# Performance work log

Hardware: AMD Instinct MI355X
Metric: run time of the kernel (lower is better)

The kernel has to match this reference:

```python
import jax, jax.numpy as jnp
import numpy as np

E, D, H, K, DIL, T = 8, 768, 3072, 3, 1, 16384


def _conv1d(x, w, b, dilation):
    # x: [1, C_in, L]; w: [C_out, C_in, K]; torch Conv1d with SAME padding
    pad = dilation * (w.shape[-1] - 1) // 2
    y = jax.lax.conv_general_dilated(
        x, w, window_strides=(1,), padding=[(pad, pad)],
        rhs_dilation=(dilation,), dimension_numbers=("NCH", "OIH", "NCH"))
    return y + b[None, :, None]


def setup_inputs() -> dict:
    key = jax.random.key(0)
    k0, k1, k2, k3, k4 = jax.random.split(key, 5)
    inp = jax.random.normal(k0, (T, D), dtype=jnp.float32)
    fwd_expert_count = jnp.full((E,), T // E, dtype=jnp.int32)
    w1 = jax.random.normal(k1, (E, H, D, K), dtype=jnp.float32) * (1.0 / np.sqrt(D * K))
    b1 = jax.random.normal(k2, (E, H), dtype=jnp.float32) * 0.01
    w2 = jax.random.normal(k3, (E, D, H, K), dtype=jnp.float32) * (1.0 / np.sqrt(H * K))
    b2 = jax.random.normal(k4, (E, D), dtype=jnp.float32) * 0.01
    return {"inp": inp, "fwd_expert_count": fwd_expert_count,
            "w1": w1, "b1": b1, "w2": w2, "b2": b2}


def reference(inp, fwd_expert_count, w1, b1, w2, b2):
    # counts define static per-expert segment lengths (constants w.r.t. compute graph)
    counts = np.asarray(jax.device_get(fwd_expert_count))
    x = inp.T[None]  # [1, D, T]
    outs, idx = [], 0
    for i in range(counts.shape[0]):
        n = int(counts[i])
        if n > 0:
            outs.append(_conv1d(x[:, :, idx:idx + n], w1[i], b1[i], DIL))
            idx += n
    h = jax.nn.gelu(jnp.concatenate(outs, axis=2), approximate=False)  # [1, H, T]
    outs, idx = [], 0
    for i in range(counts.shape[0]):
        n = int(counts[i])
        if n > 0:
            outs.append(_conv1d(h[:, :, idx:idx + n], w2[i], b2[i], DIL))
            idx += n
    y = jnp.concatenate(outs, axis=2)[0]  # [D, T]
    return y.T  # [T, D]
```

## Files before the change

kernel.cpp:

```cpp
#include <hip/hip_runtime.h>
#include <hip/hip_bf16.h>
#include <cstdint>

#define E_   8
#define D_   768
#define H_   3072
#define T_   16384
#define SEG  2048
#define PSEG (SEG + 2)

typedef __attribute__((ext_vector_type(8))) __bf16 bf16x8;
typedef __attribute__((ext_vector_type(4))) float f32x4;
typedef __attribute__((ext_vector_type(4))) unsigned int u32x4;

__device__ inline unsigned short f2bf(float f) {
  union { float f; unsigned int u; } v; v.f = f;
  unsigned int u = v.u;
  u += 0x7fffu + ((u >> 16) & 1u);
  return (unsigned short)(u >> 16);
}

__device__ inline float gelu_fast(float x) {
  const float a = -2.302118131f;
  const float b = -0.102944213f;
  float z = x * __builtin_fmaf(b, x * x, a);
  float e = __builtin_amdgcn_exp2f(z);
  return x * __builtin_amdgcn_rcpf(1.0f + e);
}

__device__ inline unsigned cvt_pk_bf16(float lo, float hi) {
  unsigned r;
  asm("v_cvt_pk_bf16_f32 %0, %1, %2" : "=v"(r) : "v"(lo), "v"(hi));
  return r;
}

__device__ inline void gload16(const unsigned short* g, unsigned short* l) {
  __builtin_amdgcn_global_load_lds(
      (const __attribute__((address_space(1))) unsigned int*)g,
      (__attribute__((address_space(3))) unsigned int*)l, 16, 0, 0);
}

__global__ __launch_bounds__(256) void cvt_x_pad_kernel(const float* __restrict__ in,
                                                        unsigned short* __restrict__ out) {
  const int i = blockIdx.x * 256 + threadIdx.x;
  const int elem = i * 8;
  const int row = elem / D_;
  const int col = elem - row * D_;
  const int prow = (row >> 11) * PSEG + 1 + (row & (SEG - 1));
  const float* p = in + (size_t)row * D_ + col;
  u32x4 v;
#pragma unroll
  for (int j = 0; j < 4; ++j)
    v[j] = (unsigned)f2bf(p[2 * j]) | ((unsigned)f2bf(p[2 * j + 1]) << 16);
  *(u32x4*)(out + (size_t)prow * D_ + col) = v;
}

__global__ __launch_bounds__(256) void zero_guards2_kernel(unsigned short* __restrict__ Xp,
                                                           unsigned short* __restrict__ Hp) {
  const int b = blockIdx.x;
  unsigned short* buf = (b < 16) ? Xp : Hp;
  const int C = (b < 16) ? D_ : H_;
  const int bb = b & 15;
  const int e = bb >> 1;
  const size_t row = (size_t)e * PSEG + (bb & 1) * (PSEG - 1);
  for (int c = threadIdx.x; c < C; c += 256) buf[row * C + c] = 0;
}

template <int C>
__global__ __launch_bounds__(256) void cvt_w_kernel(const float* __restrict__ in,
                                                    unsigned short* __restrict__ out) {
  constexpr int C8 = C / 8;
  const int i = blockIdx.x * 256 + threadIdx.x;
  const int row = i / C8;
  const int cq = i - row * C8;
  const float* src = in + ((size_t)row * C + cq * 8) * 3;
  unsigned short* dst = out + (size_t)row * 3 * C + cq * 8;
  f32x4 v[6];
#pragma unroll
  for (int j = 0; j < 6; ++j) v[j] = *(const f32x4*)(src + j * 4);
  const float* f = (const float*)v;
#pragma unroll
  for (int k = 0; k < 3; ++k) {
    u32x4 w;
#pragma unroll
    for (int j = 0; j < 4; ++j)
      w[j] = (unsigned)f2bf(f[(2 * j) * 3 + k]) |
             ((unsigned)f2bf(f[(2 * j + 1) * 3 + k]) << 16);
    *(u32x4*)(dst + k * C) = w;
  }
}

template <int CIN, int COUT, bool DO_GELU>
__global__ __launch_bounds__(512, 2) void conv_gemm8_kernel(
    const unsigned short* __restrict__ A,
    const unsigned short* __restrict__ Bt,
    const float* __restrict__ bias,
    void* __restrict__ Out) {
  __shared__ __align__(16) unsigned short lds[65536];

  constexpr int CSTEPS = CIN / 64;
  constexpr int NT = 3 * CSTEPS;
  constexpr int NTN = COUT / 256;

  const int tid  = threadIdx.x;
  const int wid  = tid >> 6, lane = tid & 63;
  const int wm   = wid >> 2, wn = wid & 3;

  const int bid = blockIdx.x;
  const int e   = bid & 7;
  const int rem = bid >> 3;
  const int mc  = rem / (4 * NTN);
  const int r2  = rem - mc * 4 * NTN;
  const int m0  = (mc * 4 + (r2 & 3)) * 256;
  const int n0  = (r2 >> 2) * 256;

  const int rowoff = tid >> 3;
  const int psrc   = ((lane & 7) ^ (lane >> 3)) * 8;
  const int ko     = (lane >> 4) * 16;
  const int ax     = (lane & 7) << 4;
  const int l15    = lane & 15;

  const int koax0 = ko ^ ax;
  const int koax1 = (64 | ko) ^ ax;
  const char* pA0 = (const char*)lds + wm * 16384 + l15 * 128 + koax0;
  const char* pA1 = (const char*)lds + wm * 16384 + l15 * 128 + koax1;
  const char* pB0 = (const char*)lds + 65536 + (wn >> 1) * 16384 +
                    ((wn & 1) * 64 + l15) * 128 + koax0;
  const char* pB1 = (const char*)lds + 65536 + (wn >> 1) * 16384 +
                    ((wn & 1) * 64 + l15) * 128 + koax1;

  const unsigned short* aU = A + ((size_t)e * PSEG + m0) * CIN;
  const unsigned short* bU = Bt + (size_t)(e * COUT + n0) * 3 * CIN;
  const int avo = rowoff * CIN + psrc;
  const int bvo = rowoff * 3 * CIN + psrc;
  size_t aOff = 0, bOff = 0;

  f32x4 acc[8][4];
#pragma unroll
  for (int n = 0; n < 4; ++n) {
    const float bv = bias[e * COUT + n0 + wn * 64 + n * 16 + l15];
#pragma unroll
    for (int m = 0; m < 8; ++m) acc[m][n] = (f32x4){bv, bv, bv, bv};
  }

#define STAGE_A(BUF_, part_) do {                                                    \
    _Pragma("unroll")                                                                \
    for (int ii_ = 0; ii_ < 2; ++ii_)                                                \
      gload16(aU + aOff + avo + (ii_ * 128 + (part_) * 64) * CIN,                    \
              (unsigned short*)((char*)lds + (BUF_) * 32768 + ii_ * 16384 +          \
                                (part_) * 8192 + wid * 1024 + lane * 16));           \
  } while (0)

#define STAGE_B(BUF_, h_) do {                                                       \
    _Pragma("unroll")                                                                \
    for (int ii_ = 0; ii_ < 2; ++ii_)                                                \
      gload16(bU + bOff + bvo + ((h_) * 128 + ii_ * 64) * 3 * CIN,                   \
              (unsigned short*)((char*)lds + 65536 + (BUF_) * 32768 + (h_) * 16384 + \
                                ii_ * 8192 + wid * 1024 + lane * 16));               \
  } while (0)

#define ADVA(nx_) do { if ((nx_) < NT) aOff += 64; } while (0)
#define ADVB(nx_) do { if ((nx_) < NT) bOff += 64; } while (0)

#define FULLBAR() do { asm volatile("" ::: "memory");                                \
                       __builtin_amdgcn_s_barrier();                                 \
                       asm volatile("" ::: "memory"); } while (0)
#define VM6() asm volatile("s_waitcnt vmcnt(6)" ::: "memory")
#define VM4() asm volatile("s_waitcnt vmcnt(4)" ::: "memory")
#define VM_NONE()

#define RA(buf_, mq_, s_, raA_, raB_, RB_) do {                                      \
    const char* pAx_ = (s_) ? pA1 : pA0;                                             \
    if (RB_) {                                                                       \
      const char* pBx_ = (s_) ? pB1 : pB0;                                           \
      _Pragma("unroll")                                                              \
      for (int n_ = 0; n_ < 4; ++n_)                                                 \
        raB_[n_] = *(const bf16x8*)(pBx_ + (buf_) * 32768 + n_ * 2048);              \
    }                                                                                \
    _Pragma("unroll")                                                                \
    for (int mi_ = 0; mi_ < 4; ++mi_)                                                \
      raA_[mi_] = *(const bf16x8*)(pAx_ + (buf_) * 32768 + ((mq_) * 4 + mi_) * 2048);\
  } while (0)

#define PHASE(raBuf_, raMq_, raS_, raA_, raB_, RB_, useA_, useB_, mq_, STAGE_STMT, VMW_) \
  do {                                                                               \
    FULLBAR();                                                                       \
    RA(raBuf_, raMq_, raS_, raA_, raB_, RB_);                                        \
    STAGE_STMT;                                                                      \
    __builtin_amdgcn_s_setprio(1);                                                   \
    _Pragma("unroll")                                                                \
    for (int mi_ = 0; mi_ < 4; ++mi_)                                                \
      _Pragma("unroll")                                                              \
      for (int n_ = 0; n_ < 4; ++n_)                                                 \
        acc[(mq_) * 4 + mi_][n_] = __builtin_amdgcn_mfma_f32_16x16x32_bf16(          \
            useA_[mi_], useB_[n_], acc[(mq_) * 4 + mi_][n_], 0, 0, 0);               \
    __builtin_amdgcn_s_setprio(0);                                                   \
    VMW_();                                                                          \
  } while (0)

  STAGE_B(0, 0); STAGE_B(0, 1); ADVB(1);
  STAGE_A(0, 0); STAGE_A(0, 1); ADVA(1);
  STAGE_B(1, 0); STAGE_B(1, 1); ADVB(2);
  VM6();
  FULLBAR();

  bf16x8 aFA[4], aFB[4], bFA[4], bFB[4];
  RA(0, 0, 0, aFA, bFA, 1);

  int kt0 = 0;
#pragma unroll 1
  for (int it = 0; it < NT / 2; ++it, kt0 += 2) {
    PHASE(0, 0, 1, aFB, bFB, 1, aFA, bFA, 0, STAGE_A(1, 0), VM6);
    PHASE(0, 1, 0, aFA, bFA, 0, aFB, bFB, 0, { STAGE_A(1, 1); ADVA(kt0 + 2); }, VM_NONE);
    PHASE(0, 1, 1, aFB, bFB, 0, aFA, bFA, 1, STAGE_B(0, 0), VM4);
    PHASE(1, 0, 0, aFA, bFA, 1, aFB, bFB, 1, { STAGE_B(0, 1); ADVB(kt0 + 3); }, VM_NONE);
    PHASE(1, 0, 1, aFB, bFB, 1, aFA, bFA, 0, STAGE_A(0, 0), VM6);
    PHASE(1, 1, 0, aFA, bFA, 0, aFB, bFB, 0, { STAGE_A(0, 1); ADVA(kt0 + 3); }, VM_NONE);
    PHASE(1, 1, 1, aFB, bFB, 0, aFA, bFA, 1, STAGE_B(1, 0), VM4);
    PHASE(0, 0, 0, aFA, bFA, 1, aFB, bFB, 1, { STAGE_B(1, 1); ADVB(kt0 + 4); }, VM_NONE);
  }

  asm volatile("s_waitcnt vmcnt(0)" ::: "memory");

#undef PHASE
#undef RA
#undef STAGE_A
#undef STAGE_B
#undef ADVA
#undef ADVB

#pragma unroll
  for (int m = 0; m < 8; ++m) {
    const int rowb = m0 + wm * 128 + m * 16 + ((lane >> 4) << 2);
#pragma unroll
    for (int n = 0; n < 4; ++n) {
      const int col = n0 + wn * 64 + n * 16 + l15;
      if (DO_GELU) {
        unsigned short* ob = (unsigned short*)Out +
                             ((size_t)e * PSEG + 1 + rowb) * COUT + col;
#pragma unroll
        for (int i = 0; i < 4; i += 2) {
          const unsigned pk = cvt_pk_bf16(gelu_fast(acc[m][n][i]),
                                          gelu_fast(acc[m][n][i + 1]));
          ob[(size_t)i * COUT] = (unsigned short)pk;
          ob[(size_t)(i + 1) * COUT] = (unsigned short)(pk >> 16);
        }
      } else {
        float* ob = (float*)Out + ((size_t)e * SEG + rowb) * COUT + col;
#pragma unroll
        for (int i = 0; i < 4; ++i) ob[(size_t)i * COUT] = acc[m][n][i];
      }
    }
  }
#undef FULLBAR
#undef VM6
#undef VM4
#undef VM_NONE
}

template <int CIN, int COUT>
__global__ __launch_bounds__(512, 2) void conv_gemm_n192_kernel(
    const unsigned short* __restrict__ A,
    const unsigned short* __restrict__ Bt,
    const float* __restrict__ bias,
    float* __restrict__ Out) {
  __shared__ __align__(16) unsigned short lds[57344];

  constexpr int CSTEPS = CIN / 64;
  constexpr int NT = 3 * CSTEPS;

  const int tid  = threadIdx.x;
  const int wid  = tid >> 6, lane = tid & 63;
  const int wm   = wid >> 2, wn = wid & 3;

  const int bid = blockIdx.x;
  const int e   = bid & 7;
  const int rem = bid >> 3;
  const int m0  = (rem & 7) * 256;
  const int n0  = (rem >> 3) * 192;

  const int rowoff = tid >> 3;
  const int psrc   = ((lane & 7) ^ (lane >> 3)) * 8;
  const int ko     = (lane >> 4) * 16;
  const int ax     = (lane & 7) << 4;
  const int l15    = lane & 15;

  const int koax0 = ko ^ ax;
  const int koax1 = (64 | ko) ^ ax;
  const char* pA0 = (const char*)lds + wm * 16384 + l15 * 128 + koax0;
  const char* pA1 = (const char*)lds + wm * 16384 + l15 * 128 + koax1;
  const char* pB0 = (const char*)lds + 65536 + wn * 6144 + l15 * 128 + koax0;
  const char* pB1 = (const char*)lds + 65536 + wn * 6144 + l15 * 128 + koax1;

  const unsigned short* aU = A + ((size_t)e * PSEG + m0) * CIN;
  const unsigned short* bU = Bt + (size_t)(e * COUT + n0) * 3 * CIN;
  const int avo = rowoff * CIN + psrc;
  const int bvo = rowoff * 3 * CIN + psrc;
  size_t aOff = 0, bOff = 0;

  f32x4 acc[8][3];
#pragma unroll
  for (int n = 0; n < 3; ++n) {
    const float bv = bias[e * COUT + n0 + wn * 48 + n * 16 + l15];
#pragma unroll
    for (int m = 0; m < 8; ++m) acc[m][n] = (f32x4){bv, bv, bv, bv};
  }

#define ADVA(nx_) do { if ((nx_) < NT) aOff += 64; } while (0)
#define ADVB(nx_) do { if ((nx_) < NT) bOff += 64; } while (0)

#define STAGE_A2(BUF_, slot_)                                                        \
  gload16(aU + aOff + avo + ((slot_) * 64) * CIN,                                    \
          (unsigned short*)((char*)lds + (BUF_) * 32768 + (slot_) * 8192 +           \
                            wid * 1024 + lane * 16))
#define STAGE_B2(BUF_, slot_)                                                        \
  gload16(bU + bOff + bvo + ((slot_) * 64) * 3 * CIN,                                \
          (unsigned short*)((char*)lds + 65536 + (BUF_) * 24576 + (slot_) * 8192 +   \
                            wid * 1024 + lane * 16))

#define FULLBAR() do { asm volatile("" ::: "memory");                                \
                       __builtin_amdgcn_s_barrier();                                 \
                       asm volatile("" ::: "memory"); } while (0)
#define VM3() asm volatile("s_waitcnt vmcnt(3)" ::: "memory")
#define VM2() asm volatile("s_waitcnt vmcnt(2)" ::: "memory")

#define RA_A2(buf_, mq_, s_, dst_) do {                                              \
    const char* pAx_ = (s_) ? pA1 : pA0;                                             \
    _Pragma("unroll")                                                                \
    for (int mi_ = 0; mi_ < 4; ++mi_)                                                \
      dst_[mi_] = *(const bf16x8*)(pAx_ + (buf_) * 32768 + ((mq_) * 4 + mi_) * 2048);\
  } while (0)

#define RA_B2(buf_, s_, dst_) do {                                                   \
    const char* pBx_ = (s_) ? pB1 : pB0;                                             \
    _Pragma("unroll")                                                                \
    for (int n_ = 0; n_ < 3; ++n_)                                                   \
      dst_[n_] = *(const bf16x8*)(pBx_ + (buf_) * 24576 + n_ * 2048);                \
  } while (0)

#define MFMA12(mq_, aU_, bU_) do {                                                   \
    __builtin_amdgcn_s_setprio(1);                                                   \
    _Pragma("unroll")                                                                \
    for (int mi_ = 0; mi_ < 4; ++mi_)                                                \
      _Pragma("unroll")                                                              \
      for (int n_ = 0; n_ < 3; ++n_)                                                 \
        acc[(mq_) * 4 + mi_][n_] = __builtin_amdgcn_mfma_f32_16x16x32_bf16(          \
            aU_[mi_], bU_[n_], acc[(mq_) * 4 + mi_][n_], 0, 0, 0);                   \
    __builtin_amdgcn_s_setprio(0);                                                   \
  } while (0)

  STAGE_A2(0, 0); STAGE_A2(0, 1); STAGE_A2(0, 2); STAGE_A2(0, 3); ADVA(1);
  STAGE_B2(0, 0); STAGE_B2(0, 1); STAGE_B2(0, 2); ADVB(1);
  STAGE_B2(1, 0); STAGE_B2(1, 1); STAGE_B2(1, 2); ADVB(2);
  VM3();
  FULLBAR();

  bf16x8 aX[4], aY[4], bF0[3], bF1[3];
  RA_A2(0, 0, 0, aX);
  RA_B2(0, 0, bF0);

  int kt0 = 0;
#pragma unroll 1
  for (int it = 0; it < NT / 2; ++it, kt0 += 2) {
    FULLBAR(); RA_A2(0, 0, 1, aY); RA_B2(0, 1, bF1);
               STAGE_A2(1, 0); STAGE_A2(1, 1); STAGE_A2(1, 2); STAGE_A2(1, 3);
               ADVA(kt0 + 2); MFMA12(0, aX, bF0);
    FULLBAR(); RA_A2(0, 1, 0, aX); MFMA12(0, aY, bF1);
    FULLBAR(); RA_A2(0, 1, 1, aY); STAGE_B2(0, 0); STAGE_B2(0, 1);
               MFMA12(1, aX, bF0); VM2();
    FULLBAR(); RA_A2(1, 0, 0, aX); RA_B2(1, 0, bF0); STAGE_B2(0, 2);
               ADVB(kt0 + 3); MFMA12(1, aY, bF1);
    FULLBAR(); RA_A2(1, 0, 1, aY); RA_B2(1, 1, bF1);
               STAGE_A2(0, 0); STAGE_A2(0, 1); STAGE_A2(0, 2); STAGE_A2(0, 3);
               ADVA(kt0 + 3); MFMA12(0, aX, bF0);
    FULLBAR(); RA_A2(1, 1, 0, aX); MFMA12(0, aY, bF1);
    FULLBAR(); RA_A2(1, 1, 1, aY); STAGE_B2(1, 0); STAGE_B2(1, 1);
               MFMA12(1, aX, bF0); VM2();
    FULLBAR(); RA_A2(0, 0, 0, aX); RA_B2(0, 0, bF0); STAGE_B2(1, 2);
               ADVB(kt0 + 4); MFMA12(1, aY, bF1);
  }

  asm volatile("s_waitcnt vmcnt(0)" ::: "memory");

#undef MFMA12
#undef RA_A2
#undef RA_B2
#undef STAGE_A2
#undef STAGE_B2
#undef ADVA
#undef ADVB
#undef FULLBAR
#undef VM3
#undef VM2

#pragma unroll
  for (int m = 0; m < 8; ++m) {
    const int rowb = m0 + wm * 128 + m * 16 + ((lane >> 4) << 2);
#pragma unroll
    for (int n = 0; n < 3; ++n) {
      const int col = n0 + wn * 48 + n * 16 + l15;
      float* ob = Out + ((size_t)e * SEG + rowb) * COUT + col;
#pragma unroll
      for (int i = 0; i < 4; ++i) ob[(size_t)i * COUT] = acc[m][n][i];
    }
  }
}

extern "C" void kernel_launch(void* const* d_in, const int* in_sizes, int n_in,
                              void* d_out, int out_size, void* d_ws, size_t ws_size,
                              hipStream_t stream) {
  const float* inp = (const float*)d_in[0];
  const float* w1 = (const float*)d_in[2];
  const float* b1 = (const float*)d_in[3];
  const float* w2 = (const float*)d_in[4];
  const float* b2 = (const float*)d_in[5];
  float* out = (float*)d_out;
  char* ws = (char*)d_ws;

  const size_t szXp = (size_t)E_ * PSEG * D_ * 2;
  const size_t szHp = (size_t)E_ * PSEG * H_ * 2;
  const size_t szW1 = (size_t)E_ * H_ * 3 * D_ * 2;
  const size_t szW2 = (size_t)E_ * D_ * 3 * H_ * 2;

  unsigned short* Xp  = (unsigned short*)ws;
  unsigned short* Hp  = (unsigned short*)(ws + szXp);
  unsigned short* W1T = (unsigned short*)(ws + szXp + szHp);
  unsigned short* W2T = (unsigned short*)(ws + szXp + szHp + szW1);

  if (ws_size < szXp + szHp + szW1 + szW2) return;

  zero_guards2_kernel<<<32, 256, 0, stream>>>(Xp, Hp);
  cvt_x_pad_kernel<<<T_ * D_ / 8 / 256, 256, 0, stream>>>(inp, Xp);
  cvt_w_kernel<D_><<<(E_ * H_) * (D_ / 8) / 256, 256, 0, stream>>>(w1, W1T);
  cvt_w_kernel<H_><<<(E_ * D_) * (H_ / 8) / 256, 256, 0, stream>>>(w2, W2T);

  constexpr int NWG1 = (H_ / 256) * (SEG / 256) * E_;
  constexpr int NWG2 = (D_ / 192) * (SEG / 256) * E_;
  conv_gemm8_kernel<D_, H_, true>
      <<<NWG1, 512, 0, stream>>>(Xp, W1T, b1, Hp);
  conv_gemm_n192_kernel<H_, D_>
      <<<NWG2, 512, 0, stream>>>(Hp, W2T, b2, out);
}
```

Measured before the change: 513.3 us.

## Switch conv GEMMs from 8-wave to 4-wave blocks with larger per-wave tiles

Result: slower. 724.4 us (+41.1%).

```diff
diff --git a/kernel.cpp b/kernel.cpp
--- a/kernel.cpp
+++ b/kernel.cpp
@@ -91,7 +91,7 @@
 }
 
 template <int CIN, int COUT, bool DO_GELU>
-__global__ __launch_bounds__(512, 2) void conv_gemm8_kernel(
+__global__ __launch_bounds__(256, 1) void conv_gemm4_kernel(
     const unsigned short* __restrict__ A,
     const unsigned short* __restrict__ Bt,
     const float* __restrict__ bias,
@@ -104,7 +104,7 @@
 
   const int tid  = threadIdx.x;
   const int wid  = tid >> 6, lane = tid & 63;
-  const int wm   = wid >> 2, wn = wid & 3;
+  const int wm   = wid >> 1, wn = wid & 1;
 
   const int bid = blockIdx.x;
   const int e   = bid & 7;
@@ -124,10 +124,8 @@
   const int koax1 = (64 | ko) ^ ax;
   const char* pA0 = (const char*)lds + wm * 16384 + l15 * 128 + koax0;
   const char* pA1 = (const char*)lds + wm * 16384 + l15 * 128 + koax1;
-  const char* pB0 = (const char*)lds + 65536 + (wn >> 1) * 16384 +
-                    ((wn & 1) * 64 + l15) * 128 + koax0;
-  const char* pB1 = (const char*)lds + 65536 + (wn >> 1) * 16384 +
-                    ((wn & 1) * 64 + l15) * 128 + koax1;
+  const char* pB0 = (const char*)lds + 65536 + wn * 16384 + l15 * 128 + koax0;
+  const char* pB1 = (const char*)lds + 65536 + wn * 16384 + l15 * 128 + koax1;
 
   const unsigned short* aU = A + ((size_t)e * PSEG + m0) * CIN;
   const unsigned short* bU = Bt + (size_t)(e * COUT + n0) * 3 * CIN;
@@ -135,10 +133,10 @@
   const int bvo = rowoff * 3 * CIN + psrc;
   size_t aOff = 0, bOff = 0;
 
-  f32x4 acc[8][4];
-#pragma unroll
-  for (int n = 0; n < 4; ++n) {
-    const float bv = bias[e * COUT + n0 + wn * 64 + n * 16 + l15];
+  f32x4 acc[8][8];
+#pragma unroll
+  for (int n = 0; n < 8; ++n) {
+    const float bv = bias[e * COUT + n0 + wn * 128 + n * 16 + l15];
 #pragma unroll
     for (int m = 0; m < 8; ++m) acc[m][n] = (f32x4){bv, bv, bv, bv};
   }
@@ -146,17 +144,23 @@
 #define STAGE_A(BUF_, part_) do {                                                    \
     _Pragma("unroll")                                                                \
     for (int ii_ = 0; ii_ < 2; ++ii_)                                                \
-      gload16(aU + aOff + avo + (ii_ * 128 + (part_) * 64) * CIN,                    \
-              (unsigned short*)((char*)lds + (BUF_) * 32768 + ii_ * 16384 +          \
-                                (part_) * 8192 + wid * 1024 + lane * 16));           \
+      _Pragma("unroll")                                                              \
+      for (int j_ = 0; j_ < 2; ++j_)                                                 \
+        gload16(aU + aOff + avo + (ii_ * 128 + (part_) * 64 + j_ * 32) * CIN,        \
+                (unsigned short*)((char*)lds + (BUF_) * 32768 + ii_ * 16384 +        \
+                                  (part_) * 8192 + j_ * 4096 + wid * 1024 +          \
+                                  lane * 16));                                       \
   } while (0)
 
 #define STAGE_B(BUF_, h_) do {                                                       \
     _Pragma("unroll")                                                                \
     for (int ii_ = 0; ii_ < 2; ++ii_)                                                \
-      gload16(bU + bOff + bvo + ((h_) * 128 + ii_ * 64) * 3 * CIN,                   \
-              (unsigned short*)((char*)lds + 65536 + (BUF_) * 32768 + (h_) * 16384 + \
-                                ii_ * 8192 + wid * 1024 + lane * 16));               \
+      _Pragma("unroll")                                                              \
+      for (int j_ = 0; j_ < 2; ++j_)                                                 \
+        gload16(bU + bOff + bvo + ((h_) * 128 + ii_ * 64 + j_ * 32) * 3 * CIN,       \
+                (unsigned short*)((char*)lds + 65536 + (BUF_) * 32768 +              \
+                                  (h_) * 16384 + ii_ * 8192 + j_ * 4096 +            \
+                                  wid * 1024 + lane * 16));                          \
   } while (0)
 
 #define ADVA(nx_) do { if ((nx_) < NT) aOff += 64; } while (0)
@@ -165,35 +169,36 @@
 #define FULLBAR() do { asm volatile("" ::: "memory");                                \
                        __builtin_amdgcn_s_barrier();                                 \
                        asm volatile("" ::: "memory"); } while (0)
-#define VM6() asm volatile("s_waitcnt vmcnt(6)" ::: "memory")
-#define VM4() asm volatile("s_waitcnt vmcnt(4)" ::: "memory")
+#define VMA() asm volatile("s_waitcnt vmcnt(12)" ::: "memory")
+#define VMB() asm volatile("s_waitcnt vmcnt(8)" ::: "memory")
 #define VM_NONE()
 
-#define RA(buf_, mq_, s_, raA_, raB_, RB_) do {                                      \
+#define RA(buf_, mh_, s_, raA_, raB_, RB_) do {                                      \
     const char* pAx_ = (s_) ? pA1 : pA0;                                             \
     if (RB_) {                                                                       \
       const char* pBx_ = (s_) ? pB1 : pB0;                                           \
       _Pragma("unroll")                                                              \
-      for (int n_ = 0; n_ < 4; ++n_)                                                 \
+      for (int n_ = 0; n_ < 8; ++n_)                                                 \
         raB_[n_] = *(const bf16x8*)(pBx_ + (buf_) * 32768 + n_ * 2048);              \
     }                                                                                \
     _Pragma("unroll")                                                                \
     for (int mi_ = 0; mi_ < 4; ++mi_)                                                \
-      raA_[mi_] = *(const bf16x8*)(pAx_ + (buf_) * 32768 + ((mq_) * 4 + mi_) * 2048);\
-  } while (0)
-
-#define PHASE(raBuf_, raMq_, raS_, raA_, raB_, RB_, useA_, useB_, mq_, STAGE_STMT, VMW_) \
+      raA_[mi_] = *(const bf16x8*)(pAx_ + (buf_) * 32768 + (mh_) * 8192 +            \
+                                   mi_ * 2048);                                      \
+  } while (0)
+
+#define PHASE(raBuf_, raMh_, raS_, raA_, raB_, RB_, useA_, useB_, mh_, STAGE_STMT, VMW_) \
   do {                                                                               \
     FULLBAR();                                                                       \
-    RA(raBuf_, raMq_, raS_, raA_, raB_, RB_);                                        \
+    RA(raBuf_, raMh_, raS_, raA_, raB_, RB_);                                        \
     STAGE_STMT;                                                                      \
     __builtin_amdgcn_s_setprio(1);                                                   \
     _Pragma("unroll")                                                                \
     for (int mi_ = 0; mi_ < 4; ++mi_)                                                \
       _Pragma("unroll")                                                              \
-      for (int n_ = 0; n_ < 4; ++n_)                                                 \
-        acc[(mq_) * 4 + mi_][n_] = __builtin_amdgcn_mfma_f32_16x16x32_bf16(          \
-            useA_[mi_], useB_[n_], acc[(mq_) * 4 + mi_][n_], 0, 0, 0);               \
+      for (int n_ = 0; n_ < 8; ++n_)                                                 \
+        acc[(mh_) * 4 + mi_][n_] = __builtin_amdgcn_mfma_f32_16x16x32_bf16(          \
+            useA_[mi_], useB_[n_], acc[(mh_) * 4 + mi_][n_], 0, 0, 0);               \
     __builtin_amdgcn_s_setprio(0);                                                   \
     VMW_();                                                                          \
   } while (0)
@@ -201,23 +206,23 @@
   STAGE_B(0, 0); STAGE_B(0, 1); ADVB(1);
   STAGE_A(0, 0); STAGE_A(0, 1); ADVA(1);
   STAGE_B(1, 0); STAGE_B(1, 1); ADVB(2);
-  VM6();
+  VMA();
   FULLBAR();
 
-  bf16x8 aFA[4], aFB[4], bFA[4], bFB[4];
-  RA(0, 0, 0, aFA, bFA, 1);
+  bf16x8 aX[4], aY[4], bF0[8], bF1[8];
+  RA(0, 0, 0, aX, bF0, 1);
 
   int kt0 = 0;
 #pragma unroll 1
   for (int it = 0; it < NT / 2; ++it, kt0 += 2) {
-    PHASE(0, 0, 1, aFB, bFB, 1, aFA, bFA, 0, STAGE_A(1, 0), VM6);
-    PHASE(0, 1, 0, aFA, bFA, 0, aFB, bFB, 0, { STAGE_A(1, 1); ADVA(kt0 + 2); }, VM_NONE);
-    PHASE(0, 1, 1, aFB, bFB, 0, aFA, bFA, 1, STAGE_B(0, 0), VM4);
-    PHASE(1, 0, 0, aFA, bFA, 1, aFB, bFB, 1, { STAGE_B(0, 1); ADVB(kt0 + 3); }, VM_NONE);
-    PHASE(1, 0, 1, aFB, bFB, 1, aFA, bFA, 0, STAGE_A(0, 0), VM6);
-    PHASE(1, 1, 0, aFA, bFA, 0, aFB, bFB, 0, { STAGE_A(0, 1); ADVA(kt0 + 3); }, VM_NONE);
-    PHASE(1, 1, 1, aFB, bFB, 0, aFA, bFA, 1, STAGE_B(1, 0), VM4);
-    PHASE(0, 0, 0, aFA, bFA, 1, aFB, bFB, 1, { STAGE_B(1, 1); ADVB(kt0 + 4); }, VM_NONE);
+    PHASE(0, 0, 1, aY, bF1, 1, aX, bF0, 0, STAGE_A(1, 0), VMA);
+    PHASE(0, 1, 0, aX, bF0, 0, aY, bF1, 0, { STAGE_A(1, 1); ADVA(kt0 + 2); }, VM_NONE);
+    PHASE(0, 1, 1, aY, bF1, 0, aX, bF0, 1, STAGE_B(0, 0), VMB);
+    PHASE(1, 0, 0, aX, bF0, 1, aY, bF1, 1, { STAGE_B(0, 1); ADVB(kt0 + 3); }, VM_NONE);
+    PHASE(1, 0, 1, aY, bF1, 1, aX, bF0, 0, STAGE_A(0, 0), VMA);
+    PHASE(1, 1, 0, aX, bF0, 0, aY, bF1, 0, { STAGE_A(0, 1); ADVA(kt0 + 3); }, VM_NONE);
+    PHASE(1, 1, 1, aY, bF1, 0, aX, bF0, 1, STAGE_B(1, 0), VMB);
+    PHASE(0, 0, 0, aX, bF0, 1, aY, bF1, 1, { STAGE_B(1, 1); ADVB(kt0 + 4); }, VM_NONE);
   }
 
   asm volatile("s_waitcnt vmcnt(0)" ::: "memory");
@@ -233,8 +238,8 @@
   for (int m = 0; m < 8; ++m) {
     const int rowb = m0 + wm * 128 + m * 16 + ((lane >> 4) << 2);
 #pragma unroll
-    for (int n = 0; n < 4; ++n) {
-      const int col = n0 + wn * 64 + n * 16 + l15;
+    for (int n = 0; n < 8; ++n) {
+      const int col = n0 + wn * 128 + n * 16 + l15;
       if (DO_GELU) {
         unsigned short* ob = (unsigned short*)Out +
                              ((size_t)e * PSEG + 1 + rowb) * COUT + col;
@@ -253,13 +258,13 @@
     }
   }
 #undef FULLBAR
-#undef VM6
-#undef VM4
+#undef VMA
+#undef VMB
 #undef VM_NONE
 }
 
 template <int CIN, int COUT>
-__global__ __launch_bounds__(512, 2) void conv_gemm_n192_kernel(
+__global__ __launch_bounds__(256, 1) void conv_gemm4_n192_kernel(
     const unsigned short* __restrict__ A,
     const unsigned short* __restrict__ Bt,
     const float* __restrict__ bias,
@@ -271,7 +276,7 @@
 
   const int tid  = threadIdx.x;
   const int wid  = tid >> 6, lane = tid & 63;
-  const int wm   = wid >> 2, wn = wid & 3;
+  const int wm   = wid >> 1, wn = wid & 1;
 
   const int bid = blockIdx.x;
   const int e   = bid & 7;
@@ -289,8 +294,8 @@
   const int koax1 = (64 | ko) ^ ax;
   const char* pA0 = (const char*)lds + wm * 16384 + l15 * 128 + koax0;
   const char* pA1 = (const char*)lds + wm * 16384 + l15 * 128 + koax1;
-  const char* pB0 = (const char*)lds + 65536 + wn * 6144 + l15 * 128 + koax0;
-  const char* pB1 = (const char*)lds + 65536 + wn * 6144 + l15 * 128 + koax1;
+  const char* pB0 = (const char*)lds + 65536 + wn * 12288 + l15 * 128 + koax0;
+  const char* pB1 = (const char*)lds + 65536 + wn * 12288 + l15 * 128 + koax1;
 
   const unsigned short* aU = A + ((size_t)e * PSEG + m0) * CIN;
   const unsigned short* bU = Bt + (size_t)(e * COUT + n0) * 3 * CIN;
@@ -298,10 +303,10 @@
   const int bvo = rowoff * 3 * CIN + psrc;
   size_t aOff = 0, bOff = 0;
 
-  f32x4 acc[8][3];
-#pragma unroll
-  for (int n = 0; n < 3; ++n) {
-    const float bv = bias[e * COUT + n0 + wn * 48 + n * 16 + l15];
+  f32x4 acc[8][6];
+#pragma unroll
+  for (int n = 0; n < 6; ++n) {
+    const float bv = bias[e * COUT + n0 + wn * 96 + n * 16 + l15];
 #pragma unroll
     for (int m = 0; m < 8; ++m) acc[m][n] = (f32x4){bv, bv, bv, bv};
   }
@@ -309,53 +314,61 @@
 #define ADVA(nx_) do { if ((nx_) < NT) aOff += 64; } while (0)
 #define ADVB(nx_) do { if ((nx_) < NT) bOff += 64; } while (0)
 
-#define STAGE_A2(BUF_, slot_)                                                        \
-  gload16(aU + aOff + avo + ((slot_) * 64) * CIN,                                    \
-          (unsigned short*)((char*)lds + (BUF_) * 32768 + (slot_) * 8192 +           \
-                            wid * 1024 + lane * 16))
-#define STAGE_B2(BUF_, slot_)                                                        \
-  gload16(bU + bOff + bvo + ((slot_) * 64) * 3 * CIN,                                \
-          (unsigned short*)((char*)lds + 65536 + (BUF_) * 24576 + (slot_) * 8192 +   \
-                            wid * 1024 + lane * 16))
+#define STAGE_A2(BUF_, slot_) do {                                                   \
+    _Pragma("unroll")                                                                \
+    for (int j_ = 0; j_ < 2; ++j_)                                                   \
+      gload16(aU + aOff + avo + ((slot_) * 64 + j_ * 32) * CIN,                      \
+              (unsigned short*)((char*)lds + (BUF_) * 32768 + (slot_) * 8192 +       \
+                                j_ * 4096 + wid * 1024 + lane * 16));                \
+  } while (0)
+#define STAGE_B2(BUF_, slot_) do {                                                   \
+    _Pragma("unroll")                                                                \
+    for (int j_ = 0; j_ < 2; ++j_)                                                   \
+      gload16(bU + bOff + bvo + ((slot_) * 64 + j_ * 32) * 3 * CIN,                  \
+              (unsigned short*)((char*)lds + 65536 + (BUF_) * 24576 +                \
+                                (slot_) * 8192 + j_ * 4096 + wid * 1024 +            \
+                                lane * 16));                                         \
+  } while (0)
 
 #define FULLBAR() do { asm volatile("" ::: "memory");                                \
                        __builtin_amdgcn_s_barrier();                                 \
                        asm volatile("" ::: "memory"); } while (0)
-#define VM3() asm volatile("s_waitcnt vmcnt(3)" ::: "memory")
-#define VM2() asm volatile("s_waitcnt vmcnt(2)" ::: "memory")
-
-#define RA_A2(buf_, mq_, s_, dst_) do {                                              \
+#define VM6() asm volatile("s_waitcnt vmcnt(6)" ::: "memory")
+#define VM4() asm volatile("s_waitcnt vmcnt(4)" ::: "memory")
+
+#define RA_A2(buf_, mh_, s_, dst_) do {                                              \
     const char* pAx_ = (s_) ? pA1 : pA0;                                             \
     _Pragma("unroll")                                                                \
     for (int mi_ = 0; mi_ < 4; ++mi_)                                                \
-      dst_[mi_] = *(const bf16x8*)(pAx_ + (buf_) * 32768 + ((mq_) * 4 + mi_) * 2048);\
+      dst_[mi_] = *(const bf16x8*)(pAx_ + (buf_) * 32768 + (mh_) * 8192 +            \
+                                   mi_ * 2048);                                      \
   } while (0)
 
 #define RA_B2(buf_, s_, dst_) do {                                                   \
     const char* pBx_ = (s_) ? pB1 : pB0;                                             \
     _Pragma("unroll")                                                                \
-    for (int n_ = 0; n_ < 3; ++n_)                                                   \
+    for (int n_ = 0; n_ < 6; ++n_)                                                   \
       dst_[n_] = *(const bf16x8*)(pBx_ + (buf_) * 24576 + n_ * 2048);                \
   } while (0)
 
-#define MFMA12(mq_, aU_, bU_) do {                                                   \
+#define MFMA24(mh_, aU_, bU_) do {                                                   \
     __builtin_amdgcn_s_setprio(1);                                                   \
     _Pragma("unroll")                                                                \
     for (int mi_ = 0; mi_ < 4; ++mi_)                                                \
       _Pragma("unroll")                                                              \
-      for (int n_ = 0; n_ < 3; ++n_)                                                 \
-        acc[(mq_) * 4 + mi_][n_] = __builtin_amdgcn_mfma_f32_16x16x32_bf16(          \
-            aU_[mi_], bU_[n_], acc[(mq_) * 4 + mi_][n_], 0, 0, 0);                   \
+      for (int n_ = 0; n_ < 6; ++n_)                                                 \
+        acc[(mh_) * 4 + mi_][n_] = __builtin_amdgcn_mfma_f32_16x16x32_bf16(          \
+            aU_[mi_], bU_[n_], acc[(mh_) * 4 + mi_][n_], 0, 0, 0);                   \
     __builtin_amdgcn_s_setprio(0);                                                   \
   } while (0)
 
   STAGE_A2(0, 0); STAGE_A2(0, 1); STAGE_A2(0, 2); STAGE_A2(0, 3); ADVA(1);
   STAGE_B2(0, 0); STAGE_B2(0, 1); STAGE_B2(0, 2); ADVB(1);
   STAGE_B2(1, 0); STAGE_B2(1, 1); STAGE_B2(1, 2); ADVB(2);
-  VM3();
+  VM6();
   FULLBAR();
 
-  bf16x8 aX[4], aY[4], bF0[3], bF1[3];
+  bf16x8 aX[4], aY[4], bF0[6], bF1[6];
   RA_A2(0, 0, 0, aX);
   RA_B2(0, 0, bF0);
 
@@ -364,25 +377,25 @@
   for (int it = 0; it < NT / 2; ++it, kt0 += 2) {
     FULLBAR(); RA_A2(0, 0, 1, aY); RA_B2(0, 1, bF1);
                STAGE_A2(1, 0); STAGE_A2(1, 1); STAGE_A2(1, 2); STAGE_A2(1, 3);
-               ADVA(kt0 + 2); MFMA12(0, aX, bF0);
-    FULLBAR(); RA_A2(0, 1, 0, aX); MFMA12(0, aY, bF1);
+               ADVA(kt0 + 2); MFMA24(0, aX, bF0);
+    FULLBAR(); RA_A2(0, 1, 0, aX); MFMA24(0, aY, bF1);
     FULLBAR(); RA_A2(0, 1, 1, aY); STAGE_B2(0, 0); STAGE_B2(0, 1);
-               MFMA12(1, aX, bF0); VM2();
+               MFMA24(1, aX, bF0); VM4();
     FULLBAR(); RA_A2(1, 0, 0, aX); RA_B2(1, 0, bF0); STAGE_B2(0, 2);
-               ADVB(kt0 + 3); MFMA12(1, aY, bF1);
+               ADVB(kt0 + 3); MFMA24(1, aY, bF1);
     FULLBAR(); RA_A2(1, 0, 1, aY); RA_B2(1, 1, bF1);
                STAGE_A2(0, 0); STAGE_A2(0, 1); STAGE_A2(0, 2); STAGE_A2(0, 3);
-               ADVA(kt0 + 3); MFMA12(0, aX, bF0);
-    FULLBAR(); RA_A2(1, 1, 0, aX); MFMA12(0, aY, bF1);
+               ADVA(kt0 + 3); MFMA24(0, aX, bF0);
+    FULLBAR(); RA_A2(1, 1, 0, aX); MFMA24(0, aY, bF1);
     FULLBAR(); RA_A2(1, 1, 1, aY); STAGE_B2(1, 0); STAGE_B2(1, 1);
-               MFMA12(1, aX, bF0); VM2();
+               MFMA24(1, aX, bF0); VM4();
     FULLBAR(); RA_A2(0, 0, 0, aX); RA_B2(0, 0, bF0); STAGE_B2(1, 2);
-               ADVB(kt0 + 4); MFMA12(1, aY, bF1);
+               ADVB(kt0 + 4); MFMA24(1, aY, bF1);
   }
 
   asm volatile("s_waitcnt vmcnt(0)" ::: "memory");
 
-#undef MFMA12
+#undef MFMA24
 #undef RA_A2
 #undef RA_B2
 #undef STAGE_A2
@@ -390,15 +403,15 @@
 #undef ADVA
 #undef ADVB
 #undef FULLBAR
-#undef VM3
-#undef VM2
+#undef VM6
+#undef VM4
 
 #pragma unroll
   for (int m = 0; m < 8; ++m) {
     const int rowb = m0 + wm * 128 + m * 16 + ((lane >> 4) << 2);
 #pragma unroll
-    for (int n = 0; n < 3; ++n) {
-      const int col = n0 + wn * 48 + n * 16 + l15;
+    for (int n = 0; n < 6; ++n) {
+      const int col = n0 + wn * 96 + n * 16 + l15;
       float* ob = Out + ((size_t)e * SEG + rowb) * COUT + col;
 #pragma unroll
       for (int i = 0; i < 4; ++i) ob[(size_t)i * COUT] = acc[m][n][i];
@@ -436,8 +449,8 @@
 
   constexpr int NWG1 = (H_ / 256) * (SEG / 256) * E_;
   constexpr int NWG2 = (D_ / 192) * (SEG / 256) * E_;
-  conv_gemm8_kernel<D_, H_, true>
-      <<<NWG1, 512, 0, stream>>>(Xp, W1T, b1, Hp);
-  conv_gemm_n192_kernel<H_, D_>
-      <<<NWG2, 512, 0, stream>>>(Hp, W2T, b2, out);
-}
+  conv_gemm4_kernel<D_, H_, true>
+      <<<NWG1, 256, 0, stream>>>(Xp, W1T, b1, Hp);
+  conv_gemm4_n192_kernel<H_, D_>
+      <<<NWG2, 256, 0, stream>>>(Hp, W2T, b2, out);
+}
```
